# Kernel optimization log

Hardware: AMD Instinct MI355X
Metric: run time of the kernel (lower is better)

The kernel has to match this reference:

```python
import jax, jax.numpy as jnp
import numpy as np

N, F, T, H, E = 50000, 8, 12, 64, 1600000

def _glorot(k, shape):
    lim = float(np.sqrt(6.0 / (shape[0] + shape[1])))
    return jax.random.uniform(k, shape, jnp.float32, -lim, lim)

def setup_inputs() -> dict:
    key = jax.random.key(0)
    ks = jax.random.split(key, 12)
    return {
        "x": jax.random.normal(ks[0], (N, F, T), jnp.float32),
        "edge_index": jax.random.randint(ks[1], (2, E), 0, N, jnp.int32),
        "edge_attr": jax.random.uniform(ks[2], (E,), jnp.float32),
        # GCNConv weights (conv_z/r/h): in_channels=F -> out_channels=H, plus bias
        "Wz": _glorot(ks[3], (F, H)), "bz": jnp.zeros((H,), jnp.float32),
        "Wr": _glorot(ks[4], (F, H)), "br": jnp.zeros((H,), jnp.float32),
        "Wh": _glorot(ks[5], (F, H)), "bh": jnp.zeros((H,), jnp.float32),
        # GRU linears: Linear(2H -> H)
        "Wlz": _glorot(ks[6], (2 * H, H)), "blz": jnp.zeros((H,), jnp.float32),
        "Wlr": _glorot(ks[7], (2 * H, H)), "blr": jnp.zeros((H,), jnp.float32),
        "Wlh": _glorot(ks[8], (2 * H, H)), "blh": jnp.zeros((H,), jnp.float32),
        # A3TGCN attention over periods
        "att": jax.random.uniform(ks[9], (T,), jnp.float32),
        # output head: Linear(H -> periods)
        "Wout": _glorot(ks[10], (H, T)), "bout": jnp.zeros((T,), jnp.float32),
    }

def _gcn_norm(edge_index, edge_attr, n):
    # GCNConv: add self-loops (weight 1), symmetric D^-1/2 (A+I) D^-1/2 normalization
    loop = jnp.arange(n, dtype=edge_index.dtype)
    src = jnp.concatenate([edge_index[0], loop])
    dst = jnp.concatenate([edge_index[1], loop])
    ew = jnp.concatenate([edge_attr, jnp.ones((n,), edge_attr.dtype)])
    deg = jax.ops.segment_sum(ew, dst, num_segments=n)
    dinv = jnp.where(deg > 0, jax.lax.rsqrt(deg), 0.0)
    return src, dst, dinv[src] * ew * dinv[dst]

def reference(x, edge_index, edge_attr, Wz, bz, Wr, br, Wh, bh,
              Wlz, blz, Wlr, blr, Wlh, blh, att, Wout, bout):
    n, _, periods = x.shape
    hid = Wz.shape[1]
    src, dst, nw = _gcn_norm(edge_index, edge_attr, n)

    def conv(xw, b):  # xw: [n, hid] features already multiplied by conv weight
        return jax.ops.segment_sum(nw[:, None] * xw[src], dst, num_segments=n) + b

    probs = jax.nn.softmax(att)
    # Upstream A3TGCN passes the SAME initial hidden (None -> zeros) to every period
    H0 = jnp.zeros((n, hid), x.dtype)
    acc = jnp.zeros((n, hid), x.dtype)
    for t in range(periods):
        xt = x[:, :, t]  # [n, F]
        Z = jax.nn.sigmoid(jnp.concatenate([conv(xt @ Wz, bz), H0], axis=1) @ Wlz + blz)
        R = jax.nn.sigmoid(jnp.concatenate([conv(xt @ Wr, br), H0], axis=1) @ Wlr + blr)
        Ht = jnp.tanh(jnp.concatenate([conv(xt @ Wh, bh), H0 * R], axis=1) @ Wlh + blh)
        acc = acc + probs[t] * (Z * H0 + (1.0 - Z) * Ht)
    h = jax.nn.relu(acc)
    return h @ Wout + bout
```

## Files before the change

kernel.cpp:

```cpp
#include <hip/hip_runtime.h>
#include <hip/hip_fp16.h>


#define NN 50000
#define EE 1600000
#define FT 96
#define TP 12
#define FF 8
#define HH 64
#define NPART 196

union Cv { ushort4 u; __half2 h[2]; };

__global__ void __launch_bounds__(256) k_init(int* counts) {
    int n = blockIdx.x * 256 + threadIdx.x;
    if (n < NN) counts[n] = 0;
}

__global__ void __launch_bounds__(256) k_count(const int* ei, int* counts, int* pos) {
    int e = blockIdx.x * 256 + threadIdx.x;
    if (e < EE) {
        int d = ei[EE + e];
        pos[e] = atomicAdd(&counts[d], 1);
    }
}

__global__ void __launch_bounds__(256) k_psum(const int* counts, int* psum) {
    __shared__ int sh[256];
    int t = threadIdx.x;
    int n = blockIdx.x * 256 + t;
    sh[t] = (n < NN) ? counts[n] : 0;
    __syncthreads();
    for (int off = 128; off > 0; off >>= 1) {
        if (t < off) sh[t] += sh[t + off];
        __syncthreads();
    }
    if (t == 0) psum[blockIdx.x] = sh[0];
}

__global__ void __launch_bounds__(256) k_ptotal(int* psum, int* rowptr) {
    __shared__ int sh[256];
    int t = threadIdx.x;
    int orig = (t < NPART) ? psum[t] : 0;
    sh[t] = orig;
    __syncthreads();
    for (int off = 1; off < 256; off <<= 1) {
        int v = (t >= off) ? sh[t - off] : 0;
        __syncthreads();
        sh[t] += v;
        __syncthreads();
    }
    if (t < NPART) psum[t] = sh[t] - orig;
    if (t == 255) rowptr[NN] = sh[255];
}

__global__ void __launch_bounds__(256) k_write(const int* counts, const int* psum,
                                               int* rowptr) {
    __shared__ int sh[256];
    int t = threadIdx.x;
    int n = blockIdx.x * 256 + t;
    int c = (n < NN) ? counts[n] : 0;
    sh[t] = c;
    __syncthreads();
    for (int off = 1; off < 256; off <<= 1) {
        int v = (t >= off) ? sh[t - off] : 0;
        __syncthreads();
        sh[t] += v;
        __syncthreads();
    }
    if (n < NN) rowptr[n] = psum[blockIdx.x] + sh[t] - c;
}

__global__ void __launch_bounds__(256) k_scatter(const int* ei, const float* ea,
                                                 const int* pos, const int* rowptr,
                                                 int2* csr) {
    int e = blockIdx.x * 256 + threadIdx.x;
    if (e < EE) {
        int s = ei[e], d = ei[EE + e];
        csr[rowptr[d] + pos[e]] = make_int2(s, __float_as_int(ea[e]));
    }
}

__global__ void __launch_bounds__(256) k_degxs(const float* __restrict__ x,
                                               const int* __restrict__ rowptr,
                                               const int2* __restrict__ csr,
                                               float* __restrict__ dinv,
                                               __half* __restrict__ xsh) {
    int wave = threadIdx.x >> 6;
    int lane = threadIdx.x & 63;
    int n = blockIdx.x * 4 + wave;
    if (n >= NN) return;
    int jb = rowptr[n], je = rowptr[n + 1];
    float s = 0.0f;
    for (int j = jb + lane; j < je; j += 64) s += __int_as_float(csr[j].y);
    for (int off = 32; off > 0; off >>= 1) s += __shfl_xor(s, off, 64);
    float di = rsqrtf(1.0f + s);
    if (lane == 0) dinv[n] = di;
    if (lane < 24) {
        float4 v = ((const float4*)(x + (size_t)n * FT))[lane];
        Cv c;
        c.h[0] = __floats2half2_rn(di * v.x, di * v.y);
        c.h[1] = __floats2half2_rn(di * v.z, di * v.w);
        ((ushort4*)xsh)[(size_t)n * 24 + lane] = c.u;
    }
}

__global__ void __launch_bounds__(64) k_fold(const float* Wz, const float* bz,
                                             const float* Wh, const float* bh,
                                             const float* Wlz, const float* blz,
                                             const float* Wlh, const float* blh,
                                             const float* att, float* fold) {
    int h = threadIdx.x;
    for (int f = 0; f < FF; f++) {
        float sz = 0.0f, sh = 0.0f;
        for (int k = 0; k < HH; k++) {
            sz += Wz[f * HH + k] * Wlz[k * HH + h];
            sh += Wh[f * HH + k] * Wlh[k * HH + h];
        }
        fold[f * HH + h]       = sz;
        fold[512 + f * HH + h] = sh;
    }
    float cz = blz[h], ch = blh[h];
    for (int k = 0; k < HH; k++) {
        cz += bz[k] * Wlz[k * HH + h];
        ch += bh[k] * Wlh[k * HH + h];
    }
    fold[1024 + h] = cz;
    fold[1088 + h] = ch;
    if (h < TP) {
        float m = -1e30f;
        for (int t = 0; t < TP; t++) m = fmaxf(m, att[t]);
        float s = 0.0f;
        for (int t = 0; t < TP; t++) s += __expf(att[t] - m);
        fold[1152 + h] = __expf(att[h] - m) / s;
    }
}

__global__ void __launch_bounds__(256) k_aggmain(const __half* __restrict__ xsh,
                                                 const float* __restrict__ dinv,
                                                 const int* __restrict__ rowptr,
                                                 const int2* __restrict__ csr,
                                                 const float* __restrict__ fold,
                                                 const float* __restrict__ Wout,
                                                 const float* __restrict__ bout,
                                                 float* __restrict__ out) {
    __shared__ float sMz[512], sMh[512], sczb[64], schb[64], sprobs[16], sWout[768], sbout[16];
    __shared__ float sy[4][FT];
    for (int i = threadIdx.x; i < 512; i += 256) { sMz[i] = fold[i]; sMh[i] = fold[512 + i]; }
    if (threadIdx.x < 64) {
        sczb[threadIdx.x] = fold[1024 + threadIdx.x];
        schb[threadIdx.x] = fold[1088 + threadIdx.x];
    }
    if (threadIdx.x < TP) {
        sprobs[threadIdx.x] = fold[1152 + threadIdx.x];
        sbout[threadIdx.x]  = bout[threadIdx.x];
    }
    for (int i = threadIdx.x; i < 768; i += 256) sWout[i] = Wout[i];

    int wave = threadIdx.x >> 6;
    int lane = threadIdx.x & 63;
    int n = blockIdx.x * 4 + wave;

    const ushort4* xsr = (const ushort4*)xsh;

    bool act = lane < 24;
    float ax = 0.0f, ay = 0.0f, az = 0.0f, aw = 0.0f;
    if (act) {
        Cv c; c.u = xsr[(size_t)n * 24 + lane];
        float2 a = __half22float2(c.h[0]);
        float2 b = __half22float2(c.h[1]);
        ax = a.x; ay = a.y; az = b.x; aw = b.y;
    }
    int jb = __builtin_amdgcn_readfirstlane(rowptr[n]);
    int je = __builtin_amdgcn_readfirstlane(rowptr[n + 1]);
    int j = jb;
    for (; j + 4 <= je; j += 4) {
        int2 m0 = csr[j];
        int2 m1 = csr[j + 1];
        int2 m2 = csr[j + 2];
        int2 m3 = csr[j + 3];
        if (act) {
            Cv c0, c1, c2, c3;
            c0.u = xsr[(size_t)m0.x * 24 + lane];
            c1.u = xsr[(size_t)m1.x * 24 + lane];
            c2.u = xsr[(size_t)m2.x * 24 + lane];
            c3.u = xsr[(size_t)m3.x * 24 + lane];
            float w0_ = __int_as_float(m0.y);
            float w1_ = __int_as_float(m1.y);
            float w2_ = __int_as_float(m2.y);
            float w3_ = __int_as_float(m3.y);
            float2 a0 = __half22float2(c0.h[0]), b0 = __half22float2(c0.h[1]);
            float2 a1 = __half22float2(c1.h[0]), b1 = __half22float2(c1.h[1]);
            float2 a2 = __half22float2(c2.h[0]), b2 = __half22float2(c2.h[1]);
            float2 a3 = __half22float2(c3.h[0]), b3 = __half22float2(c3.h[1]);
            ax = fmaf(w0_, a0.x, ax); ay = fmaf(w0_, a0.y, ay);
            az = fmaf(w0_, b0.x, az); aw = fmaf(w0_, b0.y, aw);
            ax = fmaf(w1_, a1.x, ax); ay = fmaf(w1_, a1.y, ay);
            az = fmaf(w1_, b1.x, az); aw = fmaf(w1_, b1.y, aw);
            ax = fmaf(w2_, a2.x, ax); ay = fmaf(w2_, a2.y, ay);
            az = fmaf(w2_, b2.x, az); aw = fmaf(w2_, b2.y, aw);
            ax = fmaf(w3_, a3.x, ax); ay = fmaf(w3_, a3.y, ay);
            az = fmaf(w3_, b3.x, az); aw = fmaf(w3_, b3.y, aw);
        }
    }
    for (; j < je; j++) {
        int2 m = csr[j];
        if (act) {
            Cv c; c.u = xsr[(size_t)m.x * 24 + lane];
            float wgt = __int_as_float(m.y);
            float2 a = __half22float2(c.h[0]);
            float2 b = __half22float2(c.h[1]);
            ax = fmaf(wgt, a.x, ax); ay = fmaf(wgt, a.y, ay);
            az = fmaf(wgt, b.x, az); aw = fmaf(wgt, b.y, aw);
        }
    }
    if (act) {
        float di = dinv[n];
        ((float4*)sy[wave])[lane] = make_float4(di * ax, di * ay, di * az, di * aw);
    }
    __syncthreads();

    const float* y = sy[wave];
    int h = lane;
    float zp[TP], hp[TP];
    float cz = sczb[h], ch = schb[h];
    #pragma unroll
    for (int t = 0; t < TP; t++) { zp[t] = cz; hp[t] = ch; }
    #pragma unroll
    for (int f = 0; f < FF; f++) {
        float mz = sMz[f * HH + h], mh = sMh[f * HH + h];
        #pragma unroll
        for (int t = 0; t < TP; t++) {
            float yv = y[f * TP + t];
            zp[t] = fmaf(yv, mz, zp[t]);
            hp[t] = fmaf(yv, mh, hp[t]);
        }
    }
    float acc = 0.0f;
    #pragma unroll
    for (int t = 0; t < TP; t++) {
        float z = 1.0f / (1.0f + __expf(-zp[t]));
        float hv = fmaxf(hp[t], -30.0f);
        float e = __expf(-2.0f * hv);
        float th = (1.0f - e) / (1.0f + e);
        acc += sprobs[t] * (1.0f - z) * th;
    }
    float r = fmaxf(acc, 0.0f);

    float o[TP];
    #pragma unroll
    for (int jj = 0; jj < TP; jj++) o[jj] = r * sWout[h * TP + jj];
    #pragma unroll
    for (int m = 1; m < 64; m <<= 1) {
        #pragma unroll
        for (int jj = 0; jj < TP; jj++) o[jj] += __shfl_xor(o[jj], m, 64);
    }
    if (lane == 0) {
        float* op = out + (size_t)n * TP;
        #pragma unroll
        for (int jj = 0; jj < TP; jj++) op[jj] = o[jj] + sbout[jj];
    }
}

extern "C" void kernel_launch(void* const* d_in, const int* in_sizes, int n_in,
                              void* d_out, int out_size, void* d_ws, size_t ws_size,
                              hipStream_t stream) {
    const float* x    = (const float*)d_in[0];
    const int*   ei   = (const int*)d_in[1];
    const float* ea   = (const float*)d_in[2];
    const float* Wz   = (const float*)d_in[3];
    const float* bz   = (const float*)d_in[4];
    const float* Wh   = (const float*)d_in[7];
    const float* bh   = (const float*)d_in[8];
    const float* Wlz  = (const float*)d_in[9];
    const float* blz  = (const float*)d_in[10];
    const float* Wlh  = (const float*)d_in[13];
    const float* blh  = (const float*)d_in[14];
    const float* att  = (const float*)d_in[15];
    const float* Wout = (const float*)d_in[16];
    const float* bout = (const float*)d_in[17];
    float* out = (float*)d_out;

    char* w = (char*)d_ws;
    auto alloc = [&](size_t bytes) {
        char* p = w;
        w += (bytes + 255) & ~(size_t)255;
        return p;
    };
    int*    counts = (int*)alloc(NN * 4);
    int*    rowptr = (int*)alloc((NN + 1) * 4);
    int*    pos    = (int*)alloc((size_t)EE * 4);
    int2*   csr    = (int2*)alloc((size_t)EE * 8);
    float*  dinv   = (float*)alloc(NN * 4);
    __half* xsh    = (__half*)alloc((size_t)NN * FT * 2);
    float*  fold   = (float*)alloc(2048 * 4);
    int*    psum   = (int*)alloc(NPART * 4);
    if ((size_t)(w - (char*)d_ws) > ws_size) return;

    hipLaunchKernelGGL(k_init,    dim3(NPART), dim3(256), 0, stream, counts);
    hipLaunchKernelGGL(k_count,   dim3((EE + 255) / 256), dim3(256), 0, stream, ei, counts, pos);
    hipLaunchKernelGGL(k_psum,    dim3(NPART), dim3(256), 0, stream, counts, psum);
    hipLaunchKernelGGL(k_ptotal,  dim3(1), dim3(256), 0, stream, psum, rowptr);
    hipLaunchKernelGGL(k_write,   dim3(NPART), dim3(256), 0, stream, counts, psum, rowptr);
    hipLaunchKernelGGL(k_scatter, dim3((EE + 255) / 256), dim3(256), 0, stream, ei, ea, pos, rowptr, csr);
    hipLaunchKernelGGL(k_degxs,   dim3((NN + 3) / 4), dim3(256), 0, stream, x, rowptr, csr, dinv, xsh);
    hipLaunchKernelGGL(k_fold,    dim3(1), dim3(64), 0, stream, Wz, bz, Wh, bh, Wlz, blz, Wlh, blh, att, fold);
    hipLaunchKernelGGL(k_aggmain, dim3(NN / 4), dim3(256), 0, stream,
                       xsh, dinv, rowptr, csr, fold, Wout, bout, out);
}
```

Baseline: 248.6 us.

## Gather five edges in parallel per wave with 16-byte loads and shuffle reduction

```diff
diff --git a/kernel.cpp b/kernel.cpp
--- a/kernel.cpp
+++ b/kernel.cpp
@@ -11,6 +11,7 @@
 #define NPART 196
 
 union Cv { ushort4 u; __half2 h[2]; };
+union Qv { uint4 u; __half2 h[4]; };
 
 __global__ void __launch_bounds__(256) k_init(int* counts) {
     int n = blockIdx.x * 256 + threadIdx.x;
@@ -161,71 +162,74 @@
     int lane = threadIdx.x & 63;
     int n = blockIdx.x * 4 + wave;
 
-    const ushort4* xsr = (const ushort4*)xsh;
-
-    bool act = lane < 24;
-    float ax = 0.0f, ay = 0.0f, az = 0.0f, aw = 0.0f;
-    if (act) {
-        Cv c; c.u = xsr[(size_t)n * 24 + lane];
-        float2 a = __half22float2(c.h[0]);
-        float2 b = __half22float2(c.h[1]);
-        ax = a.x; ay = a.y; az = b.x; aw = b.y;
-    }
+    const uint4* xsr = (const uint4*)xsh;
+
+    int g = lane / 12;
+    int p = lane - g * 12;
+
+    float a0 = 0.f, a1 = 0.f, a2 = 0.f, a3 = 0.f,
+          a4 = 0.f, a5 = 0.f, a6 = 0.f, a7 = 0.f;
+
+    if (g == 0) {
+        Qv q; q.u = xsr[(size_t)n * 12 + p];
+        float2 f0 = __half22float2(q.h[0]);
+        float2 f1 = __half22float2(q.h[1]);
+        float2 f2 = __half22float2(q.h[2]);
+        float2 f3 = __half22float2(q.h[3]);
+        a0 = f0.x; a1 = f0.y; a2 = f1.x; a3 = f1.y;
+        a4 = f2.x; a5 = f2.y; a6 = f3.x; a7 = f3.y;
+    }
+
     int jb = __builtin_amdgcn_readfirstlane(rowptr[n]);
     int je = __builtin_amdgcn_readfirstlane(rowptr[n + 1]);
-    int j = jb;
-    for (; j + 4 <= je; j += 4) {
-        int2 m0 = csr[j];
-        int2 m1 = csr[j + 1];
-        int2 m2 = csr[j + 2];
-        int2 m3 = csr[j + 3];
-        if (act) {
-            Cv c0, c1, c2, c3;
-            c0.u = xsr[(size_t)m0.x * 24 + lane];
-            c1.u = xsr[(size_t)m1.x * 24 + lane];
-            c2.u = xsr[(size_t)m2.x * 24 + lane];
-            c3.u = xsr[(size_t)m3.x * 24 + lane];
-            float w0_ = __int_as_float(m0.y);
-            float w1_ = __int_as_float(m1.y);
-            float w2_ = __int_as_float(m2.y);
-            float w3_ = __int_as_float(m3.y);
-            float2 a0 = __half22float2(c0.h[0]), b0 = __half22float2(c0.h[1]);
-            float2 a1 = __half22float2(c1.h[0]), b1 = __half22float2(c1.h[1]);
-            float2 a2 = __half22float2(c2.h[0]), b2 = __half22float2(c2.h[1]);
-            float2 a3 = __half22float2(c3.h[0]), b3 = __half22float2(c3.h[1]);
-            ax = fmaf(w0_, a0.x, ax); ay = fmaf(w0_, a0.y, ay);
-            az = fmaf(w0_, b0.x, az); aw = fmaf(w0_, b0.y, aw);
-            ax = fmaf(w1_, a1.x, ax); ay = fmaf(w1_, a1.y, ay);
-            az = fmaf(w1_, b1.x, az); aw = fmaf(w1_, b1.y, aw);
-            ax = fmaf(w2_, a2.x, ax); ay = fmaf(w2_, a2.y, ay);
-            az = fmaf(w2_, b2.x, az); aw = fmaf(w2_, b2.y, aw);
-            ax = fmaf(w3_, a3.x, ax); ay = fmaf(w3_, a3.y, ay);
-            az = fmaf(w3_, b3.x, az); aw = fmaf(w3_, b3.y, aw);
+    int deg = je - jb;
+
+    for (int base = 0; base < deg; base += 5) {
+        int idx = base + g;
+        bool valid = (g < 5) && (idx < deg);
+        int src = n;
+        float wgt = 0.0f;
+        if (valid) {
+            int2 m = csr[jb + idx];
+            src = m.x;
+            wgt = __int_as_float(m.y);
         }
-    }
-    for (; j < je; j++) {
-        int2 m = csr[j];
-        if (act) {
-            Cv c; c.u = xsr[(size_t)m.x * 24 + lane];
-            float wgt = __int_as_float(m.y);
-            float2 a = __half22float2(c.h[0]);
-            float2 b = __half22float2(c.h[1]);
-            ax = fmaf(wgt, a.x, ax); ay = fmaf(wgt, a.y, ay);
-            az = fmaf(wgt, b.x, az); aw = fmaf(wgt, b.y, aw);
-        }
-    }
-    if (act) {
+        Qv q; q.u = xsr[(size_t)src * 12 + p];
+        float2 f0 = __half22float2(q.h[0]);
+        float2 f1 = __half22float2(q.h[1]);
+        float2 f2 = __half22float2(q.h[2]);
+        float2 f3 = __half22float2(q.h[3]);
+        a0 = fmaf(wgt, f0.x, a0); a1 = fmaf(wgt, f0.y, a1);
+        a2 = fmaf(wgt, f1.x, a2); a3 = fmaf(wgt, f1.y, a3);
+        a4 = fmaf(wgt, f2.x, a4); a5 = fmaf(wgt, f2.y, a5);
+        a6 = fmaf(wgt, f3.x, a6); a7 = fmaf(wgt, f3.y, a7);
+    }
+
+    {
+        float t0, t1, t2, t3;
+        #define RED(A) \
+            t0 = __shfl(A, lane + 12, 64); \
+            t1 = __shfl(A, lane + 24, 64); \
+            t2 = __shfl(A, lane + 36, 64); \
+            t3 = __shfl(A, lane + 48, 64); \
+            A = A + t0 + t1 + t2 + t3;
+        RED(a0) RED(a1) RED(a2) RED(a3) RED(a4) RED(a5) RED(a6) RED(a7)
+        #undef RED
+    }
+
+    if (lane < 12) {
         float di = dinv[n];
-        ((float4*)sy[wave])[lane] = make_float4(di * ax, di * ay, di * az, di * aw);
+        ((float4*)sy[wave])[2 * lane]     = make_float4(di * a0, di * a1, di * a2, di * a3);
+        ((float4*)sy[wave])[2 * lane + 1] = make_float4(di * a4, di * a5, di * a6, di * a7);
     }
     __syncthreads();
 
     const float* y = sy[wave];
     int h = lane;
     float zp[TP], hp[TP];
-    float cz = sczb[h], ch = schb[h];
-    #pragma unroll
-    for (int t = 0; t < TP; t++) { zp[t] = cz; hp[t] = ch; }
+    float cz = sczb[h], chb = schb[h];
+    #pragma unroll
+    for (int t = 0; t < TP; t++) { zp[t] = cz; hp[t] = chb; }
     #pragma unroll
     for (int f = 0; f < FF; f++) {
         float mz = sMz[f * HH + h], mh = sMh[f * HH + h];
```

Measured after the change: 247.1 us. Within noise of the previous version (-0.6%).
